# Performance work log

Hardware: AMD Instinct MI355X
Metric: run time of the kernel (lower is better)

Reference implementation:

```python
import jax, jax.numpy as jnp
import numpy as np

F_NUM, D_IN, D_OUT, H = 64, 256, 256, 8
LN_EPS = 1e-5


def setup_inputs() -> dict:
    key = jax.random.key(0)
    ks = jax.random.split(key, 7)
    B = 1024
    dh = D_OUT // H
    # xavier_normal_ with gain 1.414 on [F, d, w]: std = gain*sqrt(2/(fan_in+fan_out)),
    # torch treats dim0 as batch-of-matrices only for 2D; for 3D fan_in=d*w? Use simple
    # gaussian init scaled like xavier over the last two dims (values irrelevant to math).
    std_qkv = 1.414 * np.sqrt(2.0 / (D_IN + D_OUT))
    std_lin = 1.414 * np.sqrt(2.0 / (D_IN + D_OUT))
    std_w = 1.414 * np.sqrt(2.0 / (1 + dh))
    return {
        "theta": jax.random.normal(ks[0], (B, F_NUM, D_IN), jnp.float32),
        "Q": jax.random.normal(ks[1], (F_NUM, D_IN, D_OUT), jnp.float32) * std_qkv,
        "K": jax.random.normal(ks[2], (F_NUM, D_IN, D_OUT), jnp.float32) * std_qkv,
        "V": jax.random.normal(ks[3], (F_NUM, D_IN, D_OUT), jnp.float32) * std_qkv,
        "W_lin": jax.random.normal(ks[4], (D_OUT, D_IN), jnp.float32) * std_lin,  # Linear weight [out,in]
        "rot_w": jax.random.normal(ks[5], (1, dh), jnp.float32) * std_w,
        "ln_gamma": jnp.ones((D_OUT,), jnp.float32),
        "ln_beta": jnp.zeros((D_OUT,), jnp.float32),
    }


def _split_heads(x, H):
    B, F, W = x.shape
    return x.reshape(B, F, H, W // H).transpose(0, 2, 1, 3)  # [B,H,F,dh]


def reference(theta, Q, K, V, W_lin, rot_w, ln_gamma, ln_beta):
    B = theta.shape[0]
    t = theta.reshape(B, -1, D_IN)  # [B,F,d]
    q = jnp.einsum('bfd,fdw->bfw', t, Q)
    k = jnp.einsum('bfd,fdw->bfw', t, K)
    v = jnp.einsum('bfd,fdw->bfw', t, V)
    q, k, v = _split_heads(q, H), _split_heads(k, H), _split_heads(v, H)  # [B,H,F,dh]
    cos_a = jnp.cos(q) * rot_w
    sin_a = jnp.sin(q) * rot_w
    logits = (jnp.einsum('bhfe,bhge->bhfg', cos_a, jnp.cos(k))
              + jnp.einsum('bhfe,bhge->bhfg', sin_a, jnp.sin(k)))
    S = jax.nn.sigmoid(logits)  # [B,H,F,F] (query f, key g)
    # (dropout p=0 -> identity)
    out = jnp.einsum('bhfg,bhgd->bhfd', S, v)  # [B,H,F,dh]
    out = out.transpose(0, 2, 1, 3).reshape(B, F_NUM, D_OUT)  # concat heads in order
    res = out + jnp.einsum('bfd,wd->bfw', theta, W_lin)
    mu = jnp.mean(res, axis=-1, keepdims=True)
    var = jnp.mean((res - mu) ** 2, axis=-1, keepdims=True)
    normed = (res - mu) * jax.lax.rsqrt(var + LN_EPS)
    return normed * ln_gamma + ln_beta
```

## Files before the change

kernel.cpp:

```cpp
#include <hip/hip_runtime.h>

typedef __attribute__((ext_vector_type(8))) short bf16x8;
typedef __attribute__((ext_vector_type(8))) unsigned short u16x8;
typedef __attribute__((ext_vector_type(4))) unsigned short u16x4;
typedef __attribute__((ext_vector_type(4))) float f32x4;
typedef unsigned short u16;

__device__ __forceinline__ float b2f(u16 u) {
    return __builtin_bit_cast(float, (unsigned)u << 16);
}
__device__ __forceinline__ u16 f2b(float f) {
    unsigned i = __builtin_bit_cast(unsigned, f);
    return (u16)((i + 0x7FFFu + ((i >> 16) & 1u)) >> 16);
}

__global__ __launch_bounds__(256) void wtrans_kernel(
    const float* __restrict__ Q, const float* __restrict__ K, const float* __restrict__ V,
    u16* __restrict__ WT)
{
    int z = blockIdx.z; int m = z >> 6, f = z & 63;
    const float* src = (m == 0 ? Q : (m == 1 ? K : V)) + (size_t)f * 65536;
    u16* dst = WT + (size_t)z * 65536;
    int w0 = blockIdx.x * 64, d0 = blockIdx.y * 64;
    __shared__ u16 tile[64][68];
    int tid = threadIdx.x;
#pragma unroll
    for (int i = 0; i < 2; ++i) {
        int idx = tid * 2 + i; int r = idx >> 3; int c8 = (idx & 7) * 8;
        const float* p = src + (size_t)(d0 + r) * 256 + w0 + c8;
        f32x4 a = *(const f32x4*)p, b = *(const f32x4*)(p + 4);
        u16x4 lo, hi;
#pragma unroll
        for (int j = 0; j < 4; ++j) { lo[j] = f2b(a[j]); hi[j] = f2b(b[j]); }
        *(u16x4*)&tile[r][c8] = lo;
        *(u16x4*)&tile[r][c8 + 4] = hi;
    }
    __syncthreads();
#pragma unroll
    for (int i = 0; i < 2; ++i) {
        int idx = tid * 2 + i; int rw = idx >> 3; int c8 = (idx & 7) * 8;
        u16x8 v;
#pragma unroll
        for (int j = 0; j < 8; ++j) v[j] = tile[c8 + j][rw];
        *(u16x8*)(dst + (size_t)(w0 + rw) * 256 + d0 + c8) = v;
    }
}

__global__ __launch_bounds__(256) void qkv_gemm_kernel(
    const float* __restrict__ theta, const u16* __restrict__ WT, u16* __restrict__ ws, int B)
{
    int z = blockIdx.z; int m = z >> 6, f = z & 63;
    const float* A = theta + (size_t)f * 256;
    const u16* Bt = WT + (size_t)z * 65536;
    u16* C = ws + (size_t)m * B * 16384 + (size_t)f * 256;
    int bm0 = blockIdx.x * 128, bn0 = blockIdx.y * 128;
    __shared__ u16 As[128][32];
    __shared__ u16 Bs[128][32];
    int tid = threadIdx.x, wave = tid >> 6, lane = tid & 63;
    int l15 = lane & 15, quad = lane >> 4;
    int wm0 = (wave >> 1) * 64, wn0 = (wave & 1) * 64;
    f32x4 acc[4][4];
#pragma unroll
    for (int mi = 0; mi < 4; ++mi)
#pragma unroll
        for (int ni = 0; ni < 4; ++ni) acc[mi][ni] = f32x4{0.f, 0.f, 0.f, 0.f};
    for (int k0 = 0; k0 < 256; k0 += 32) {
#pragma unroll
        for (int i = 0; i < 2; ++i) {
            int idx = tid * 2 + i; int r = idx >> 2; int c8 = (idx & 3) * 8;
            const float* p = A + (size_t)(bm0 + r) * 16384 + k0 + c8;
            f32x4 a = *(const f32x4*)p, b = *(const f32x4*)(p + 4);
            u16x8 v;
#pragma unroll
            for (int j = 0; j < 4; ++j) { v[j] = f2b(a[j]); v[j + 4] = f2b(b[j]); }
            *(u16x8*)&As[r][c8] = v;
            *(u16x8*)&Bs[r][c8] = *(const u16x8*)(Bt + (size_t)(bn0 + r) * 256 + k0 + c8);
        }
        __syncthreads();
        bf16x8 af[4], bfr[4];
#pragma unroll
        for (int mi = 0; mi < 4; ++mi) af[mi] = *(const bf16x8*)&As[wm0 + mi * 16 + l15][quad * 8];
#pragma unroll
        for (int ni = 0; ni < 4; ++ni) bfr[ni] = *(const bf16x8*)&Bs[wn0 + ni * 16 + l15][quad * 8];
#pragma unroll
        for (int mi = 0; mi < 4; ++mi)
#pragma unroll
            for (int ni = 0; ni < 4; ++ni)
                acc[mi][ni] = __builtin_amdgcn_mfma_f32_16x16x32_bf16(af[mi], bfr[ni], acc[mi][ni], 0, 0, 0);
        __syncthreads();
    }
#pragma unroll
    for (int mi = 0; mi < 4; ++mi)
#pragma unroll
        for (int ni = 0; ni < 4; ++ni)
#pragma unroll
            for (int r = 0; r < 4; ++r)
                C[(size_t)(bm0 + wm0 + mi * 16 + quad * 4 + r) * 16384 + bn0 + wn0 + ni * 16 + l15] =
                    f2b(acc[mi][ni][r]);
}

__global__ __launch_bounds__(256) void attn_kernel(
    const u16* __restrict__ qws, const u16* __restrict__ kws, const u16* __restrict__ vws,
    float* __restrict__ attf, const float* __restrict__ rotw)
{
    int b = blockIdx.x;
    int tid = threadIdx.x, wave = tid >> 6, lane = tid & 63;
    int l15 = lane & 15, quad = lane >> 4;
    __shared__ u16 Sb[4][64][72];
    __shared__ u16 Vb[4][64][32];
    const size_t base = (size_t)b * (64 * 256);
    float rw[8];
    {
        f32x4 r0 = *(const f32x4*)(rotw + quad * 8);
        f32x4 r1 = *(const f32x4*)(rotw + quad * 8 + 4);
#pragma unroll
        for (int j = 0; j < 4; ++j) { rw[j] = r0[j]; rw[j + 4] = r1[j]; }
    }
    for (int hi = 0; hi < 2; ++hi) {
        int h = wave + hi * 4;
        const u16* qh = qws + base + h * 32;
        const u16* kh = kws + base + h * 32;
        const u16* vh = vws + base + h * 32;
#pragma unroll
        for (int i = 0; i < 4; ++i) {
            int row = i * 16 + (lane >> 2); int c8 = (lane & 3) * 8;
            *(u16x8*)&Vb[wave][row][c8] = *(const u16x8*)(vh + (size_t)row * 256 + c8);
        }
        bf16x8 af[4][2], bfr[4][2];
#pragma unroll
        for (int mi = 0; mi < 4; ++mi) {
            u16x8 q8 = *(const u16x8*)(qh + (size_t)(mi * 16 + l15) * 256 + quad * 8);
            bf16x8 c, s;
#pragma unroll
            for (int j = 0; j < 8; ++j) {
                float v = b2f(q8[j]);
                c[j] = (short)f2b(__cosf(v) * rw[j]);
                s[j] = (short)f2b(__sinf(v) * rw[j]);
            }
            af[mi][0] = c; af[mi][1] = s;
        }
#pragma unroll
        for (int ni = 0; ni < 4; ++ni) {
            u16x8 k8 = *(const u16x8*)(kh + (size_t)(ni * 16 + l15) * 256 + quad * 8);
            bf16x8 c, s;
#pragma unroll
            for (int j = 0; j < 8; ++j) {
                float v = b2f(k8[j]);
                c[j] = (short)f2b(__cosf(v));
                s[j] = (short)f2b(__sinf(v));
            }
            bfr[ni][0] = c; bfr[ni][1] = s;
        }
        f32x4 acc[4][4];
#pragma unroll
        for (int mi = 0; mi < 4; ++mi)
#pragma unroll
            for (int ni = 0; ni < 4; ++ni) acc[mi][ni] = f32x4{0.f, 0.f, 0.f, 0.f};
#pragma unroll
        for (int kc = 0; kc < 2; ++kc)
#pragma unroll
            for (int mi = 0; mi < 4; ++mi)
#pragma unroll
                for (int ni = 0; ni < 4; ++ni)
                    acc[mi][ni] = __builtin_amdgcn_mfma_f32_16x16x32_bf16(af[mi][kc], bfr[ni][kc], acc[mi][ni], 0, 0, 0);
#pragma unroll
        for (int mi = 0; mi < 4; ++mi)
#pragma unroll
            for (int ni = 0; ni < 4; ++ni)
#pragma unroll
                for (int r = 0; r < 4; ++r) {
                    float x = acc[mi][ni][r];
                    float sg = __builtin_amdgcn_rcpf(1.f + __expf(-x));
                    Sb[wave][mi * 16 + quad * 4 + r][ni * 16 + l15] = f2b(sg);
                }
        f32x4 ao[4][2];
#pragma unroll
        for (int mi = 0; mi < 4; ++mi)
#pragma unroll
            for (int n2 = 0; n2 < 2; ++n2) ao[mi][n2] = f32x4{0.f, 0.f, 0.f, 0.f};
#pragma unroll
        for (int kc = 0; kc < 2; ++kc) {
            bf16x8 pb[2];
#pragma unroll
            for (int n2 = 0; n2 < 2; ++n2)
#pragma unroll
                for (int j = 0; j < 8; ++j)
                    pb[n2][j] = (short)Vb[wave][kc * 32 + quad * 8 + j][n2 * 16 + l15];
#pragma unroll
            for (int mi = 0; mi < 4; ++mi) {
                bf16x8 pa = *(const bf16x8*)&Sb[wave][mi * 16 + l15][kc * 32 + quad * 8];
#pragma unroll
                for (int n2 = 0; n2 < 2; ++n2)
                    ao[mi][n2] = __builtin_amdgcn_mfma_f32_16x16x32_bf16(pa, pb[n2], ao[mi][n2], 0, 0, 0);
            }
        }
#pragma unroll
        for (int mi = 0; mi < 4; ++mi)
#pragma unroll
            for (int n2 = 0; n2 < 2; ++n2)
#pragma unroll
                for (int r = 0; r < 4; ++r)
                    attf[base + (size_t)(mi * 16 + quad * 4 + r) * 256 + h * 32 + n2 * 16 + l15] =
                        ao[mi][n2][r];
    }
}

__global__ __launch_bounds__(512) void lin_ln_kernel(
    const float* __restrict__ theta, const float* __restrict__ Wl, const float* att,
    const float* __restrict__ gamma, const float* __restrict__ beta, float* out)
{
    int tid = threadIdx.x, wave = tid >> 6, lane = tid & 63;
    int l15 = lane & 15, quad = lane >> 4;
    int bm0 = blockIdx.x * 128;
    int wm0 = (wave >> 2) * 64, wn0 = (wave & 3) * 64;
    int wn = wave & 3;
    __shared__ u16 As[128][32];
    __shared__ u16 Bs[256][32];
    __shared__ float red1[128][4];
    __shared__ float red2[128][4];
    f32x4 acc[4][4];
#pragma unroll
    for (int mi = 0; mi < 4; ++mi)
#pragma unroll
        for (int ni = 0; ni < 4; ++ni) acc[mi][ni] = f32x4{0.f, 0.f, 0.f, 0.f};
    for (int k0 = 0; k0 < 256; k0 += 32) {
        {
            int r = tid >> 2; int c8 = (tid & 3) * 8;
            const float* p = theta + (size_t)(bm0 + r) * 256 + k0 + c8;
            f32x4 a = *(const f32x4*)p, b = *(const f32x4*)(p + 4);
            u16x8 v;
#pragma unroll
            for (int j = 0; j < 4; ++j) { v[j] = f2b(a[j]); v[j + 4] = f2b(b[j]); }
            *(u16x8*)&As[r][c8] = v;
        }
#pragma unroll
        for (int i = 0; i < 2; ++i) {
            int idx = tid * 2 + i; int r = idx >> 2; int c8 = (idx & 3) * 8;
            const float* p = Wl + (size_t)r * 256 + k0 + c8;
            f32x4 a = *(const f32x4*)p, b = *(const f32x4*)(p + 4);
            u16x8 v;
#pragma unroll
            for (int j = 0; j < 4; ++j) { v[j] = f2b(a[j]); v[j + 4] = f2b(b[j]); }
            *(u16x8*)&Bs[r][c8] = v;
        }
        __syncthreads();
        bf16x8 af[4], bfr[4];
#pragma unroll
        for (int mi = 0; mi < 4; ++mi) af[mi] = *(const bf16x8*)&As[wm0 + mi * 16 + l15][quad * 8];
#pragma unroll
        for (int ni = 0; ni < 4; ++ni) bfr[ni] = *(const bf16x8*)&Bs[wn0 + ni * 16 + l15][quad * 8];
#pragma unroll
        for (int mi = 0; mi < 4; ++mi)
#pragma unroll
            for (int ni = 0; ni < 4; ++ni)
                acc[mi][ni] = __builtin_amdgcn_mfma_f32_16x16x32_bf16(af[mi], bfr[ni], acc[mi][ni], 0, 0, 0);
        __syncthreads();
    }
    float gam[4], bet[4];
#pragma unroll
    for (int ni = 0; ni < 4; ++ni) {
        gam[ni] = gamma[wn0 + ni * 16 + l15];
        bet[ni] = beta[wn0 + ni * 16 + l15];
    }
#pragma unroll
    for (int mi = 0; mi < 4; ++mi)
#pragma unroll
        for (int ni = 0; ni < 4; ++ni)
#pragma unroll
            for (int r = 0; r < 4; ++r)
                acc[mi][ni][r] += att[(size_t)(bm0 + wm0 + mi * 16 + quad * 4 + r) * 256 + wn0 + ni * 16 + l15];
#pragma unroll
    for (int mi = 0; mi < 4; ++mi)
#pragma unroll
        for (int r = 0; r < 4; ++r) {
            float s1 = 0.f, s2 = 0.f;
#pragma unroll
            for (int ni = 0; ni < 4; ++ni) { float x = acc[mi][ni][r]; s1 += x; s2 += x * x; }
#pragma unroll
            for (int off = 1; off < 16; off <<= 1) {
                s1 += __shfl_xor(s1, off);
                s2 += __shfl_xor(s2, off);
            }
            if (l15 == 0) {
                int lr = wm0 + mi * 16 + quad * 4 + r;
                red1[lr][wn] = s1; red2[lr][wn] = s2;
            }
        }
    __syncthreads();
#pragma unroll
    for (int mi = 0; mi < 4; ++mi)
#pragma unroll
        for (int r = 0; r < 4; ++r) {
            int lr = wm0 + mi * 16 + quad * 4 + r;
            float s1 = red1[lr][0] + red1[lr][1] + red1[lr][2] + red1[lr][3];
            float s2 = red2[lr][0] + red2[lr][1] + red2[lr][2] + red2[lr][3];
            float mu = s1 * (1.f / 256.f);
            float var = s2 * (1.f / 256.f) - mu * mu;
            float inv = rsqrtf(var + 1e-5f);
#pragma unroll
            for (int ni = 0; ni < 4; ++ni) {
                float y = (acc[mi][ni][r] - mu) * inv * gam[ni] + bet[ni];
                out[(size_t)(bm0 + lr) * 256 + wn0 + ni * 16 + l15] = y;
            }
        }
}

extern "C" void kernel_launch(void* const* d_in, const int* in_sizes, int n_in,
                              void* d_out, int out_size, void* d_ws, size_t ws_size,
                              hipStream_t stream)
{
    const float* theta = (const float*)d_in[0];
    const float* Q  = (const float*)d_in[1];
    const float* K  = (const float*)d_in[2];
    const float* V  = (const float*)d_in[3];
    const float* Wl = (const float*)d_in[4];
    const float* rotw = (const float*)d_in[5];
    const float* gam = (const float*)d_in[6];
    const float* bet = (const float*)d_in[7];
    int B = in_sizes[0] / (64 * 256);
    u16* ws = (u16*)d_ws;
    size_t per = (size_t)B * 16384;
    u16* wsq = ws;
    u16* wsk = ws + per;
    u16* wsv = ws + 2 * per;
    u16* wT  = ws + 3 * per;
    float* outf = (float*)d_out;

    wtrans_kernel<<<dim3(4, 4, 192), 256, 0, stream>>>(Q, K, V, wT);
    qkv_gemm_kernel<<<dim3(B / 128, 2, 192), 256, 0, stream>>>(theta, wT, ws, B);
    attn_kernel<<<dim3(B), 256, 0, stream>>>(wsq, wsk, wsv, outf, rotw);
    lin_ln_kernel<<<dim3(B * 64 / 128), 512, 0, stream>>>(theta, Wl, outf, gam, bet, outf);
}
```

Before: 312.2 us.

## Reuse theta A-tile across Q/K/V GEMMs with async double-buffered B loads

The QKV GEMM kernel now loads and converts each 128x256 theta tile to bf16 once, keeps all of its A fragments in registers, and loops over the Q, K and V weight matrices in a single block. This cuts the grid from 192 to 64 in z. B tiles are streamed through double-buffered LDS using global_load_lds async copies, and the A staging uses an XOR swizzle to avoid bank conflicts. The aim is to remove the threefold re-read and re-conversion of theta and to overlap B loads with MFMA. The cost is higher register pressure (32 A fragments per thread under launch_bounds(256,2)) and fewer, longer blocks.

```diff
diff --git a/kernel.cpp b/kernel.cpp
--- a/kernel.cpp
+++ b/kernel.cpp
@@ -12,6 +12,10 @@
 __device__ __forceinline__ u16 f2b(float f) {
     unsigned i = __builtin_bit_cast(unsigned, f);
     return (u16)((i + 0x7FFFu + ((i >> 16) & 1u)) >> 16);
+}
+__device__ __forceinline__ void async_cp16(const u16* g, u16* l) {
+    __builtin_amdgcn_global_load_lds((const __attribute__((address_space(1))) void*)g,
+                                     (__attribute__((address_space(3))) void*)l, 16, 0, 0);
 }
 
 __global__ __launch_bounds__(256) void wtrans_kernel(
@@ -46,57 +50,85 @@
     }
 }
 
-__global__ __launch_bounds__(256) void qkv_gemm_kernel(
+__global__ __launch_bounds__(256, 2) void qkv_gemm_kernel(
     const float* __restrict__ theta, const u16* __restrict__ WT, u16* __restrict__ ws, int B)
 {
-    int z = blockIdx.z; int m = z >> 6, f = z & 63;
-    const float* A = theta + (size_t)f * 256;
-    const u16* Bt = WT + (size_t)z * 65536;
-    u16* C = ws + (size_t)m * B * 16384 + (size_t)f * 256;
+    int f = blockIdx.z;
     int bm0 = blockIdx.x * 128, bn0 = blockIdx.y * 128;
-    __shared__ u16 As[128][32];
-    __shared__ u16 Bs[128][32];
+    __shared__ u16 smem[32768];
     int tid = threadIdx.x, wave = tid >> 6, lane = tid & 63;
     int l15 = lane & 15, quad = lane >> 4;
     int wm0 = (wave >> 1) * 64, wn0 = (wave & 1) * 64;
+
+    const float* Af = theta + (size_t)f * 256;
+#pragma unroll
+    for (int p = 0; p < 16; ++p) {
+        int id = p * 256 + tid;
+        int r = id >> 5, c = id & 31;
+        const float* g = Af + (size_t)(bm0 + r) * 16384 + c * 8;
+        f32x4 a = *(const f32x4*)g, b = *(const f32x4*)(g + 4);
+        u16x8 v;
+#pragma unroll
+        for (int j = 0; j < 4; ++j) { v[j] = f2b(a[j]); v[j + 4] = f2b(b[j]); }
+        *(u16x8*)&smem[r * 256 + ((c ^ (r & 7)) * 8)] = v;
+    }
+    __syncthreads();
+    bf16x8 af[4][8];
+#pragma unroll
+    for (int mi = 0; mi < 4; ++mi)
+#pragma unroll
+        for (int kk = 0; kk < 8; ++kk) {
+            int row = wm0 + mi * 16 + l15;
+            int pos = (kk * 4 + quad) ^ (l15 & 7);
+            af[mi][kk] = *(const bf16x8*)&smem[row * 256 + pos * 8];
+        }
+    __syncthreads();
+
+    auto issueB = [&](int it) {
+        int m = it >> 3, kk = it & 7, buf = it & 1;
+        const u16* Bt = WT + (size_t)(m * 64 + f) * 65536;
+#pragma unroll
+        for (int i = 0; i < 2; ++i) {
+            int r0 = wave * 32 + i * 16;
+            const u16* g = Bt + (size_t)(bn0 + r0 + (lane >> 2)) * 256 + kk * 32 + (lane & 3) * 8;
+            async_cp16(g, &smem[buf * 4096 + r0 * 32]);
+        }
+    };
+    issueB(0);
     f32x4 acc[4][4];
 #pragma unroll
-    for (int mi = 0; mi < 4; ++mi)
-#pragma unroll
-        for (int ni = 0; ni < 4; ++ni) acc[mi][ni] = f32x4{0.f, 0.f, 0.f, 0.f};
-    for (int k0 = 0; k0 < 256; k0 += 32) {
-#pragma unroll
-        for (int i = 0; i < 2; ++i) {
-            int idx = tid * 2 + i; int r = idx >> 2; int c8 = (idx & 3) * 8;
-            const float* p = A + (size_t)(bm0 + r) * 16384 + k0 + c8;
-            f32x4 a = *(const f32x4*)p, b = *(const f32x4*)(p + 4);
-            u16x8 v;
-#pragma unroll
-            for (int j = 0; j < 4; ++j) { v[j] = f2b(a[j]); v[j + 4] = f2b(b[j]); }
-            *(u16x8*)&As[r][c8] = v;
-            *(u16x8*)&Bs[r][c8] = *(const u16x8*)(Bt + (size_t)(bn0 + r) * 256 + k0 + c8);
+    for (int it = 0; it < 24; ++it) {
+        int kk = it & 7, buf = it & 1;
+        if (kk == 0) {
+#pragma unroll
+            for (int mi = 0; mi < 4; ++mi)
+#pragma unroll
+                for (int ni = 0; ni < 4; ++ni) acc[mi][ni] = f32x4{0.f, 0.f, 0.f, 0.f};
         }
         __syncthreads();
-        bf16x8 af[4], bfr[4];
-#pragma unroll
-        for (int mi = 0; mi < 4; ++mi) af[mi] = *(const bf16x8*)&As[wm0 + mi * 16 + l15][quad * 8];
-#pragma unroll
-        for (int ni = 0; ni < 4; ++ni) bfr[ni] = *(const bf16x8*)&Bs[wn0 + ni * 16 + l15][quad * 8];
+        if (it < 23) issueB(it + 1);
+        bf16x8 bfr[4];
+#pragma unroll
+        for (int ni = 0; ni < 4; ++ni)
+            bfr[ni] = *(const bf16x8*)&smem[buf * 4096 + (wn0 + ni * 16 + l15) * 32 + quad * 8];
 #pragma unroll
         for (int mi = 0; mi < 4; ++mi)
 #pragma unroll
             for (int ni = 0; ni < 4; ++ni)
-                acc[mi][ni] = __builtin_amdgcn_mfma_f32_16x16x32_bf16(af[mi], bfr[ni], acc[mi][ni], 0, 0, 0);
-        __syncthreads();
-    }
-#pragma unroll
-    for (int mi = 0; mi < 4; ++mi)
-#pragma unroll
-        for (int ni = 0; ni < 4; ++ni)
-#pragma unroll
-            for (int r = 0; r < 4; ++r)
-                C[(size_t)(bm0 + wm0 + mi * 16 + quad * 4 + r) * 16384 + bn0 + wn0 + ni * 16 + l15] =
-                    f2b(acc[mi][ni][r]);
+                acc[mi][ni] = __builtin_amdgcn_mfma_f32_16x16x32_bf16(af[mi][kk], bfr[ni], acc[mi][ni], 0, 0, 0);
+        if (kk == 7) {
+            int m = it >> 3;
+            u16* C = ws + (size_t)m * B * 16384 + (size_t)f * 256;
+#pragma unroll
+            for (int mi = 0; mi < 4; ++mi)
+#pragma unroll
+                for (int ni = 0; ni < 4; ++ni)
+#pragma unroll
+                    for (int r = 0; r < 4; ++r)
+                        C[(size_t)(bm0 + wm0 + mi * 16 + quad * 4 + r) * 16384 + bn0 + wn0 + ni * 16 + l15] =
+                            f2b(acc[mi][ni][r]);
+        }
+    }
 }
 
 __global__ __launch_bounds__(256) void attn_kernel(
@@ -327,7 +359,7 @@
     float* outf = (float*)d_out;
 
     wtrans_kernel<<<dim3(4, 4, 192), 256, 0, stream>>>(Q, K, V, wT);
-    qkv_gemm_kernel<<<dim3(B / 128, 2, 192), 256, 0, stream>>>(theta, wT, ws, B);
+    qkv_gemm_kernel<<<dim3(B / 128, 2, 64), 256, 0, stream>>>(theta, wT, ws, B);
     attn_kernel<<<dim3(B), 256, 0, stream>>>(wsq, wsk, wsv, outf, rotw);
     lin_ln_kernel<<<dim3(B * 64 / 128), 512, 0, stream>>>(theta, Wl, outf, gam, bet, outf);
 }
```

After: 289.9 us. -7.2%, faster.
